# Kernel optimization log

Hardware: AMD Instinct MI355X
Metric: run time of the kernel (lower is better)

## Reference

```python
import jax, jax.numpy as jnp
import numpy as np

HEADS = 8
GROUPS = 32
EPS = 1e-5


def setup_inputs() -> dict:
    key = jax.random.key(0)
    k_x, k_qkv, k_proj = jax.random.split(key, 3)
    B, C, H, W = 16, 512, 32, 32
    s = 0.02  # init scale for weights
    return {
        "x": jax.random.normal(k_x, (B, C, H, W), jnp.float32),
        "gn_scale": jnp.ones((C,), jnp.float32),
        "gn_bias": jnp.zeros((C,), jnp.float32),
        "w_qkv": jax.random.normal(k_qkv, (3 * C, C), jnp.float32) * s,
        "b_qkv": jnp.zeros((3 * C,), jnp.float32),
        "w_proj": jax.random.normal(k_proj, (C, C), jnp.float32) * s,
        "b_proj": jnp.zeros((C,), jnp.float32),
    }


def _group_norm(x, scale, bias):
    # x: [B, C, T]; GroupNorm32 computes stats in fp32
    B, C, T = x.shape
    xg = x.reshape(B, GROUPS, C // GROUPS, T).astype(jnp.float32)
    mu = xg.mean(axis=(2, 3), keepdims=True)
    var = xg.var(axis=(2, 3), keepdims=True)
    xn = ((xg - mu) * jax.lax.rsqrt(var + EPS)).reshape(B, C, T)
    return xn * scale[None, :, None] + bias[None, :, None]


def reference(x, gn_scale, gn_bias, w_qkv, b_qkv, w_proj, b_proj):
    B, C = x.shape[0], x.shape[1]
    T = int(np.prod(x.shape[2:]))
    xf = x.reshape(B, C, T)
    xn = _group_norm(xf, gn_scale, gn_bias).astype(x.dtype)
    # 1x1 conv == per-position matmul: [B, 3C, T]
    qkv = jnp.einsum('oc,bct->bot', w_qkv, xn) + b_qkv[None, :, None]
    ch = C // HEADS
    qkv = qkv.reshape(B * HEADS, 3 * ch, T)
    q, k, v = jnp.split(qkv, 3, axis=1)  # each [B*H, ch, T]
    scale = ch ** -0.25
    # scores: [B*H, T, T], softmax in fp32 (matches weight.float())
    w = jnp.einsum('bct,bcs->bts', q * scale, k * scale)
    w = jax.nn.softmax(w.astype(jnp.float32), axis=-1).astype(q.dtype)
    a = jnp.einsum('bts,bcs->bct', w, v).reshape(B, C, T)
    h = jnp.einsum('oc,bct->bot', w_proj, a) + b_proj[None, :, None]
    return (xf + h).reshape(x.shape)
```

## Files before the change

### kernel.cpp

```cpp
#include <hip/hip_runtime.h>
#include <cstdint>

#define NB 16
#define NC 512
#define NT 1024
#define NH 8
#define NG 32
#define GN_EPS 1e-5f
#define KSOFT 0.18033688011112042f

typedef float  f32x16 __attribute__((ext_vector_type(16)));
typedef __bf16 bf16x8 __attribute__((ext_vector_type(8)));
typedef unsigned int uint32x4 __attribute__((ext_vector_type(4)));

static __device__ __forceinline__ f32x16 zero16() {
    f32x16 z;
    #pragma unroll
    for (int i = 0; i < 16; ++i) z[i] = 0.f;
    return z;
}

static __device__ __forceinline__ f32x16 mfma(bf16x8 a, bf16x8 b, f32x16 c) {
    return __builtin_amdgcn_mfma_f32_32x32x16_bf16(a, b, c, 0, 0, 0);
}

static __device__ __forceinline__ unsigned pk2(float a, float b) {
    unsigned short x = __builtin_bit_cast(unsigned short, (__bf16)a);
    unsigned short y = __builtin_bit_cast(unsigned short, (__bf16)b);
    return (unsigned)x | ((unsigned)y << 16);
}

static __device__ __forceinline__ void swap32(unsigned& a, unsigned& b) {
#if __has_builtin(__builtin_amdgcn_permlane32_swap)
    auto r = __builtin_amdgcn_permlane32_swap(a, b, false, false);
    a = r[0];
    b = r[1];
#else
    unsigned sa = __shfl_xor(a, 32), sb = __shfl_xor(b, 32);
    bool hi = (threadIdx.x & 32) != 0;
    unsigned na = hi ? sb : a;
    unsigned nb = hi ? b : sa;
    a = na; b = nb;
#endif
}

static __device__ __forceinline__ bf16x8 lds_frag(const __bf16* base, int row, int sb) {
    const char* p = (const char*)base + row * 128 + (sb ^ ((row & 7) << 4));
    return *(const bf16x8*)p;
}

#define GLOAD16(gp, lp)                                                        \
    __builtin_amdgcn_global_load_lds(                                          \
        (const __attribute__((address_space(1))) unsigned int*)(gp),           \
        (__attribute__((address_space(3))) unsigned int*)(lp), 16, 0, 0)

__global__ __launch_bounds__(256) void fused_pre(
        const float* __restrict__ x, const float* __restrict__ gs,
        const float* __restrict__ gb, const float* __restrict__ w_qkv,
        const float* __restrict__ w_proj, __bf16* __restrict__ xnT,
        __bf16* __restrict__ wq_bf, __bf16* __restrict__ wp_bf)
{
    const int blk = blockIdx.x;
    const int thr = threadIdx.x;
    if (blk >= 128) {
        int i = (blk - 128) * 256 + thr;
        const float* src;
        __bf16* dst;
        if (i < 196608) { src = w_qkv; dst = wq_bf; }
        else            { i -= 196608; src = w_proj; dst = wp_bf; }
        float4 f = ((const float4*)src)[i];
        uint2 u;
        u.x = pk2(f.x, f.y);
        u.y = pk2(f.z, f.w);
        ((uint2*)dst)[i] = u;
        return;
    }
    const int b = blk >> 3, c0 = (blk & 7) * 64;
    __shared__ float gstat[8];
    {
        const int wv = thr >> 6, lane = thr & 63;
        const float* base = x + ((size_t)b * NC + c0 + wv * 16) * NT;
        float s = 0.f, s2 = 0.f;
        #pragma unroll
        for (int ch = 0; ch < 16; ++ch) {
            const float4* r4 = (const float4*)(base + (size_t)ch * NT);
            #pragma unroll
            for (int p = 0; p < 4; ++p) {
                float4 v = r4[lane + p * 64];
                s += v.x + v.y + v.z + v.w;
                s2 = fmaf(v.x, v.x, fmaf(v.y, v.y, fmaf(v.z, v.z, fmaf(v.w, v.w, s2))));
            }
        }
        #pragma unroll
        for (int off = 32; off; off >>= 1) {
            s  += __shfl_down(s, off);
            s2 += __shfl_down(s2, off);
        }
        if (lane == 0) {
            const float inv_n = 1.f / 16384.f;
            float mu  = s * inv_n;
            float var = s2 * inv_n - mu * mu;
            gstat[wv]     = mu;
            gstat[wv + 4] = rsqrtf(var + GN_EPS);
        }
    }
    __syncthreads();
    __shared__ float xs[64][65];
    const int tloc = thr & 63;
    for (int t0 = 0; t0 < NT; t0 += 64) {
        #pragma unroll
        for (int p = 0; p < 16; ++p) {
            int cr = p * 4 + (thr >> 6);
            int c = c0 + cr;
            float mu = gstat[cr >> 4];
            float rs = gstat[(cr >> 4) + 4];
            float v = x[((size_t)b * NC + c) * NT + t0 + tloc];
            xs[cr][tloc] = (v - mu) * rs * gs[c] + gb[c];
        }
        __syncthreads();
        const int cd = thr & 31;
        #pragma unroll
        for (int pp = 0; pp < 8; ++pp) {
            int tr = pp * 8 + (thr >> 5);
            unsigned w = pk2(xs[2 * cd][tr], xs[2 * cd + 1][tr]);
            size_t off = ((size_t)b * NT + t0 + tr) * NC + c0 + 2 * cd;
            *(unsigned*)((char*)xnT + off * 2) = w;
        }
        __syncthreads();
    }
}

__global__ __launch_bounds__(256) void qkv_gemm(const __bf16* __restrict__ wq,
                                                const __bf16* __restrict__ xnT,
                                                const float* __restrict__ bias,
                                                __bf16* __restrict__ qv,
                                                __bf16* __restrict__ kT)
{
    const int b = blockIdx.z, o0 = blockIdx.y * 128, t0 = blockIdx.x * 128;
    __shared__ __align__(16) char smem[32768];
    __bf16* wt = (__bf16*)smem;
    __bf16* xt = (__bf16*)(smem + 16384);
    const int thr = threadIdx.x;
    const int lane = thr & 63, wv = thr >> 6;
    const int lr = lane & 31, h = lane >> 5;
    const int wo = (wv >> 1) * 64, wn = (wv & 1) * 64;
    f32x16 acc[2][2];
    #pragma unroll
    for (int i = 0; i < 2; ++i)
        #pragma unroll
        for (int j = 0; j < 2; ++j) acc[i][j] = zero16();

    for (int kb = 0; kb < 8; ++kb) {
        const int c0 = kb * 64;
        __syncthreads();
        #pragma unroll
        for (int p = 0; p < 4; ++p) {
            int idx = p * 256 + thr, row = idx >> 3, sl = idx & 7;
            GLOAD16(wq + (size_t)(o0 + row) * NC + c0 + 8 * (sl ^ (row & 7)), wt + idx * 8);
            GLOAD16(xnT + ((size_t)b * NT + t0 + row) * NC + c0 + 8 * (sl ^ (row & 7)), xt + idx * 8);
        }
        asm volatile("s_waitcnt vmcnt(0)" ::: "memory");
        __syncthreads();
        #pragma unroll
        for (int kc = 0; kc < 4; ++kc) {
            bf16x8 a0 = lds_frag(wt, wo + lr,      32 * kc + 16 * h);
            bf16x8 a1 = lds_frag(wt, wo + 32 + lr, 32 * kc + 16 * h);
            bf16x8 b0 = lds_frag(xt, wn + lr,      32 * kc + 16 * h);
            bf16x8 b1 = lds_frag(xt, wn + 32 + lr, 32 * kc + 16 * h);
            acc[0][0] = mfma(a0, b0, acc[0][0]);
            acc[0][1] = mfma(a0, b1, acc[0][1]);
            acc[1][0] = mfma(a1, b0, acc[1][0]);
            acc[1][1] = mfma(a1, b1, acc[1][1]);
        }
    }

    char* ktile = smem;
    #pragma unroll
    for (int mt = 0; mt < 2; ++mt) {
        const int X = o0 + wo + 32 * mt;
        const int xm = X % 192;
        const int cat = xm >> 6;
        const int hd = X / 192;
        if (cat != 1) {
            #pragma unroll
            for (int nt = 0; nt < 2; ++nt)
                #pragma unroll
                for (int r = 0; r < 16; ++r) {
                    int off = (r & 3) + 8 * (r >> 2) + 4 * h;
                    int o = X + off;
                    int row = (cat == 0) ? (xm + off) : (xm - 64 + off);
                    int t = t0 + wn + 32 * nt + lr;
                    float v = acc[mt][nt][r] + bias[o];
                    if (cat == 0) v *= KSOFT;
                    qv[((size_t)(b * 8 + hd) * 128 + row) * NT + t] = (__bf16)v;
                }
        }
    }
    __syncthreads();
    #pragma unroll
    for (int mt = 0; mt < 2; ++mt) {
        const int X = o0 + wo + 32 * mt;
        const int xm = X % 192;
        if ((xm >> 6) == 1) {
            #pragma unroll
            for (int nt = 0; nt < 2; ++nt) {
                int t_local = wn + 32 * nt + lr;
                #pragma unroll
                for (int g = 0; g < 4; ++g) {
                    int ob = X + 8 * g + 4 * h;
                    int cb = (xm - 64) + 8 * g + 4 * h;
                    uint2 d;
                    d.x = pk2(acc[mt][nt][4 * g + 0] + bias[ob + 0],
                              acc[mt][nt][4 * g + 1] + bias[ob + 1]);
                    d.y = pk2(acc[mt][nt][4 * g + 2] + bias[ob + 2],
                              acc[mt][nt][4 * g + 3] + bias[ob + 3]);
                    *(uint2*)(ktile + t_local * 144 + cb * 2) = d;
                }
            }
        }
    }
    if ((o0 % 192) != 128) {
        __syncthreads();
        const int khd = o0 / 192;
        #pragma unroll
        for (int pass = 0; pass < 4; ++pass) {
            int t_local = pass * 32 + (thr >> 3);
            int c8 = thr & 7;
            uint32x4 d = *(const uint32x4*)(ktile + t_local * 144 + c8 * 16);
            *(uint32x4*)(kT + ((size_t)(b * 8 + khd) * 1024 + t0 + t_local) * 64 + c8 * 8) = d;
        }
    }
}

#define PP(R) ((R) < 16 ? p0[(R) & 15] : p1[(R) & 15])

__global__ __launch_bounds__(512, 4) void attn_mfma(const __bf16* __restrict__ qv,
                                                    const __bf16* __restrict__ kT,
                                                    __bf16* __restrict__ aT)
{
    const int wg = blockIdx.x;
    const int orig = (wg & 7) * 64 + (wg >> 3);
    const int tq0 = (orig & 3) * 256;
    const int bh = orig >> 2;
    const int b = bh >> 3, hd = bh & 7;
    const __bf16* qg = qv + (size_t)bh * 128 * NT;
    const __bf16* vg = qg + (size_t)64 * NT;
    const __bf16* kTg = kT + (size_t)bh * 1024 * 64;
    const int thr = threadIdx.x, lane = thr & 63, wv = thr >> 6;
    const int lr = lane & 31, h = lane >> 5;
    const int tw = tq0 + wv * 32;
    __shared__ __align__(16) char smem[36864];
    __bf16* kb0 = (__bf16*)smem;
    __bf16* vb0 = (__bf16*)(smem + 8192);
    __bf16* kb1 = (__bf16*)(smem + 16384);
    __bf16* vb1 = (__bf16*)(smem + 24576);

    bf16x8 qf[4];
    {
        const unsigned short* qs = (const unsigned short*)qg;
        #pragma unroll
        for (int kc = 0; kc < 4; ++kc) {
            unsigned w[4];
            #pragma unroll
            for (int ww = 0; ww < 4; ++ww) {
                int c0 = 16 * kc + 8 * h + 2 * ww;
                unsigned lo = qs[(size_t)c0 * NT + tw + lr];
                unsigned hi = qs[(size_t)(c0 + 1) * NT + tw + lr];
                w[ww] = lo | (hi << 16);
            }
            uint32x4 u = {w[0], w[1], w[2], w[3]};
            qf[kc] = __builtin_bit_cast(bf16x8, u);
        }
    }
    bf16x8 ones;
    #pragma unroll
    for (int i = 0; i < 8; ++i) ones[i] = (__bf16)1.0f;

    f32x16 oacc0 = zero16(), oacc1 = zero16(), sacc = zero16();

    const int row = thr >> 3, sl = thr & 7;
    const __bf16* kbase = kTg + (size_t)row * 64 + 8 * (sl ^ (row & 7));
    const __bf16* vbase = vg + (size_t)row * NT + 8 * (sl ^ (row & 7));
    const int ldsoff = thr * 8;

    GLOAD16(kbase, kb0 + ldsoff);
    GLOAD16(vbase, vb0 + ldsoff);

    for (int it = 0; it < 16; ++it) {
        __bf16* kcur = (it & 1) ? kb1 : kb0;
        __bf16* vcur = (it & 1) ? vb1 : vb0;
        if (it < 15) {
            __bf16* knxt = (it & 1) ? kb0 : kb1;
            __bf16* vnxt = (it & 1) ? vb0 : vb1;
            const int s0 = (it + 1) * 64;
            GLOAD16(kbase + (size_t)s0 * 64, knxt + ldsoff);
            GLOAD16(vbase + s0, vnxt + ldsoff);
            asm volatile("s_waitcnt vmcnt(2)" ::: "memory");
        } else {
            asm volatile("s_waitcnt vmcnt(0)" ::: "memory");
        }
        __builtin_amdgcn_s_barrier();

        f32x16 p0 = zero16(), p1 = zero16();
        __builtin_amdgcn_s_setprio(1);
        #pragma unroll
        for (int kc = 0; kc < 4; ++kc) {
            bf16x8 ka0 = lds_frag(kcur, lr,      32 * kc + 16 * h);
            bf16x8 ka1 = lds_frag(kcur, 32 + lr, 32 * kc + 16 * h);
            p0 = mfma(ka0, qf[kc], p0);
            p1 = mfma(ka1, qf[kc], p1);
        }
        __builtin_amdgcn_s_setprio(0);

        #pragma unroll
        for (int r = 0; r < 16; ++r) {
            p0[r] = exp2f(p0[r]);
            p1[r] = exp2f(p1[r]);
        }

        #pragma unroll
        for (int ks = 0; ks < 4; ++ks) {
            const int Rb = 16 * (ks >> 1) + 8 * (ks & 1);
            unsigned a0 = pk2(PP(Rb + 0), PP(Rb + 1));
            unsigned c0 = pk2(PP(Rb + 2), PP(Rb + 3));
            unsigned a1 = pk2(PP(Rb + 4), PP(Rb + 5));
            unsigned c1 = pk2(PP(Rb + 6), PP(Rb + 7));
            swap32(a0, a1);
            swap32(c0, c1);
            uint32x4 u = {a0, c0, a1, c1};
            bf16x8 pf = __builtin_bit_cast(bf16x8, u);
            bf16x8 v0 = lds_frag(vcur, lr,      32 * ks + 16 * h);
            bf16x8 v1 = lds_frag(vcur, 32 + lr, 32 * ks + 16 * h);
            __builtin_amdgcn_s_setprio(1);
            oacc0 = mfma(v0, pf, oacc0);
            oacc1 = mfma(v1, pf, oacc1);
            sacc  = mfma(ones, pf, sacc);
            __builtin_amdgcn_s_setprio(0);
        }
        __builtin_amdgcn_s_barrier();
    }

    float inv = 1.f / sacc[0];
    char* at = smem;
    {
        int t_local = wv * 32 + lr;
        #pragma unroll
        for (int g = 0; g < 4; ++g) {
            int cb = 8 * g + 4 * h;
            uint2 d0, d1;
            d0.x = pk2(oacc0[4 * g + 0] * inv, oacc0[4 * g + 1] * inv);
            d0.y = pk2(oacc0[4 * g + 2] * inv, oacc0[4 * g + 3] * inv);
            *(uint2*)(at + t_local * 144 + cb * 2) = d0;
            d1.x = pk2(oacc1[4 * g + 0] * inv, oacc1[4 * g + 1] * inv);
            d1.y = pk2(oacc1[4 * g + 2] * inv, oacc1[4 * g + 3] * inv);
            *(uint2*)(at + t_local * 144 + (cb + 32) * 2) = d1;
        }
    }
    __syncthreads();
    #pragma unroll
    for (int pass = 0; pass < 4; ++pass) {
        int t_local = pass * 64 + (thr >> 3);
        int c8 = thr & 7;
        uint32x4 d = *(const uint32x4*)(at + t_local * 144 + c8 * 16);
        *(uint32x4*)(aT + ((size_t)b * NT + tq0 + t_local) * NC + hd * 64 + c8 * 8) = d;
    }
}

__global__ __launch_bounds__(256) void proj_gemm(const __bf16* __restrict__ wp,
                                                 const __bf16* __restrict__ aT,
                                                 const float* __restrict__ bias,
                                                 const float* __restrict__ x,
                                                 float* __restrict__ out)
{
    const int b = blockIdx.z, o0 = blockIdx.y * 128, t0 = blockIdx.x * 128;
    __shared__ __align__(16) char smem[32768];
    __bf16* wt = (__bf16*)smem;
    __bf16* xt = (__bf16*)(smem + 16384);
    const int thr = threadIdx.x;
    const int lane = thr & 63, wv = thr >> 6;
    const int lr = lane & 31, h = lane >> 5;
    const int wo = (wv >> 1) * 64, wn = (wv & 1) * 64;
    f32x16 acc[2][2];
    #pragma unroll
    for (int i = 0; i < 2; ++i)
        #pragma unroll
        for (int j = 0; j < 2; ++j) acc[i][j] = zero16();

    for (int kb = 0; kb < 8; ++kb) {
        const int c0 = kb * 64;
        __syncthreads();
        #pragma unroll
        for (int p = 0; p < 4; ++p) {
            int idx = p * 256 + thr, row = idx >> 3, sl = idx & 7;
            GLOAD16(wp + (size_t)(o0 + row) * NC + c0 + 8 * (sl ^ (row & 7)), wt + idx * 8);
            GLOAD16(aT + ((size_t)b * NT + t0 + row) * NC + c0 + 8 * (sl ^ (row & 7)), xt + idx * 8);
        }
        asm volatile("s_waitcnt vmcnt(0)" ::: "memory");
        __syncthreads();
        #pragma unroll
        for (int kc = 0; kc < 4; ++kc) {
            bf16x8 a0 = lds_frag(wt, wo + lr,      32 * kc + 16 * h);
            bf16x8 a1 = lds_frag(wt, wo + 32 + lr, 32 * kc + 16 * h);
            bf16x8 b0 = lds_frag(xt, wn + lr,      32 * kc + 16 * h);
            bf16x8 b1 = lds_frag(xt, wn + 32 + lr, 32 * kc + 16 * h);
            acc[0][0] = mfma(a0, b0, acc[0][0]);
            acc[0][1] = mfma(a0, b1, acc[0][1]);
            acc[1][0] = mfma(a1, b0, acc[1][0]);
            acc[1][1] = mfma(a1, b1, acc[1][1]);
        }
    }
    #pragma unroll
    for (int mt = 0; mt < 2; ++mt)
        #pragma unroll
        for (int nt = 0; nt < 2; ++nt)
            #pragma unroll
            for (int r = 0; r < 16; ++r) {
                int o = o0 + wo + 32 * mt + (r & 3) + 8 * (r >> 2) + 4 * h;
                int t = t0 + wn + 32 * nt + lr;
                size_t off = ((size_t)b * NC + o) * NT + t;
                out[off] = acc[mt][nt][r] + bias[o] + x[off];
            }
}

extern "C" void kernel_launch(void* const* d_in, const int* in_sizes, int n_in,
                              void* d_out, int out_size, void* d_ws, size_t ws_size,
                              hipStream_t stream)
{
    const float* x       = (const float*)d_in[0];
    const float* gnscale = (const float*)d_in[1];
    const float* gnbias  = (const float*)d_in[2];
    const float* w_qkv   = (const float*)d_in[3];
    const float* b_qkv   = (const float*)d_in[4];
    const float* w_proj  = (const float*)d_in[5];
    const float* b_proj  = (const float*)d_in[6];
    float* out = (float*)d_out;

    char* ws = (char*)d_ws;
    __bf16* wq_bf = (__bf16*)(ws + 4096);
    __bf16* wp_bf = (__bf16*)(ws + 1576960);
    __bf16* xnT   = (__bf16*)(ws + 2101248);
    __bf16* qv    = (__bf16*)(ws + 18878464);
    __bf16* kTb   = (__bf16*)(ws + 52432896);
    __bf16* aTb   = (__bf16*)(ws + 69210112);

    fused_pre<<<1152, 256, 0, stream>>>(x, gnscale, gnbias, w_qkv, w_proj,
                                        xnT, wq_bf, wp_bf);
    qkv_gemm<<<dim3(8, 12, NB), 256, 0, stream>>>(wq_bf, xnT, b_qkv, qv, kTb);
    attn_mfma<<<512, 512, 0, stream>>>(qv, kTb, aTb);
    proj_gemm<<<dim3(8, 4, NB), 256, 0, stream>>>(wp_bf, aTb, b_proj, x, out);
}
```

Before: 143.4 us.

## Double-buffer LDS tiles in QKV and projection GEMMs to overlap loads with MFMA

Both the QKV and output-projection GEMM kernels now keep two 32KB LDS stages. While the current k-block is computed, the next one is prefetched, and a partial vmcnt wait is used instead of a full drain, so global-to-LDS load latency is meant to hide behind MFMA work. This doubles LDS use to 64KB per block, which may cut occupancy. It also depends on the vmcnt(8) count matching the number of outstanding loads for correctness.

```diff
diff --git a/kernel.cpp b/kernel.cpp
--- a/kernel.cpp
+++ b/kernel.cpp
@@ -137,9 +137,7 @@
                                                 __bf16* __restrict__ kT)
 {
     const int b = blockIdx.z, o0 = blockIdx.y * 128, t0 = blockIdx.x * 128;
-    __shared__ __align__(16) char smem[32768];
-    __bf16* wt = (__bf16*)smem;
-    __bf16* xt = (__bf16*)(smem + 16384);
+    __shared__ __align__(16) char smem[65536];
     const int thr = threadIdx.x;
     const int lane = thr & 63, wv = thr >> 6;
     const int lr = lane & 31, h = lane >> 5;
@@ -150,17 +148,31 @@
         #pragma unroll
         for (int j = 0; j < 2; ++j) acc[i][j] = zero16();
 
+#define QKV_STAGE(c0v, wbuf, xbuf)                                             \
+    {                                                                          \
+        _Pragma("unroll")                                                      \
+        for (int p = 0; p < 4; ++p) {                                          \
+            int idx = p * 256 + thr, row = idx >> 3, sl = idx & 7;             \
+            GLOAD16(wq + (size_t)(o0 + row) * NC + (c0v) + 8 * (sl ^ (row & 7)), (wbuf) + idx * 8); \
+            GLOAD16(xnT + ((size_t)b * NT + t0 + row) * NC + (c0v) + 8 * (sl ^ (row & 7)), (xbuf) + idx * 8); \
+        }                                                                      \
+    }
+
+    QKV_STAGE(0, (__bf16*)smem, (__bf16*)(smem + 16384));
+
     for (int kb = 0; kb < 8; ++kb) {
-        const int c0 = kb * 64;
-        __syncthreads();
-        #pragma unroll
-        for (int p = 0; p < 4; ++p) {
-            int idx = p * 256 + thr, row = idx >> 3, sl = idx & 7;
-            GLOAD16(wq + (size_t)(o0 + row) * NC + c0 + 8 * (sl ^ (row & 7)), wt + idx * 8);
-            GLOAD16(xnT + ((size_t)b * NT + t0 + row) * NC + c0 + 8 * (sl ^ (row & 7)), xt + idx * 8);
-        }
-        asm volatile("s_waitcnt vmcnt(0)" ::: "memory");
-        __syncthreads();
+        const int cur = kb & 1;
+        __bf16* wt = (__bf16*)(smem + cur * 32768);
+        __bf16* xt = (__bf16*)(smem + cur * 32768 + 16384);
+        if (kb < 7) {
+            __bf16* wn2 = (__bf16*)(smem + (cur ^ 1) * 32768);
+            __bf16* xn2 = (__bf16*)(smem + (cur ^ 1) * 32768 + 16384);
+            QKV_STAGE((kb + 1) * 64, wn2, xn2);
+            asm volatile("s_waitcnt vmcnt(8)" ::: "memory");
+        } else {
+            asm volatile("s_waitcnt vmcnt(0)" ::: "memory");
+        }
+        __builtin_amdgcn_s_barrier();
         #pragma unroll
         for (int kc = 0; kc < 4; ++kc) {
             bf16x8 a0 = lds_frag(wt, wo + lr,      32 * kc + 16 * h);
@@ -172,6 +184,7 @@
             acc[1][0] = mfma(a1, b0, acc[1][0]);
             acc[1][1] = mfma(a1, b1, acc[1][1]);
         }
+        __builtin_amdgcn_s_barrier();
     }
 
     char* ktile = smem;
@@ -373,9 +386,7 @@
                                                  float* __restrict__ out)
 {
     const int b = blockIdx.z, o0 = blockIdx.y * 128, t0 = blockIdx.x * 128;
-    __shared__ __align__(16) char smem[32768];
-    __bf16* wt = (__bf16*)smem;
-    __bf16* xt = (__bf16*)(smem + 16384);
+    __shared__ __align__(16) char smem[65536];
     const int thr = threadIdx.x;
     const int lane = thr & 63, wv = thr >> 6;
     const int lr = lane & 31, h = lane >> 5;
@@ -386,17 +397,31 @@
         #pragma unroll
         for (int j = 0; j < 2; ++j) acc[i][j] = zero16();
 
+#define PROJ_STAGE(c0v, wbuf, xbuf)                                            \
+    {                                                                          \
+        _Pragma("unroll")                                                      \
+        for (int p = 0; p < 4; ++p) {                                          \
+            int idx = p * 256 + thr, row = idx >> 3, sl = idx & 7;             \
+            GLOAD16(wp + (size_t)(o0 + row) * NC + (c0v) + 8 * (sl ^ (row & 7)), (wbuf) + idx * 8); \
+            GLOAD16(aT + ((size_t)b * NT + t0 + row) * NC + (c0v) + 8 * (sl ^ (row & 7)), (xbuf) + idx * 8); \
+        }                                                                      \
+    }
+
+    PROJ_STAGE(0, (__bf16*)smem, (__bf16*)(smem + 16384));
+
     for (int kb = 0; kb < 8; ++kb) {
-        const int c0 = kb * 64;
-        __syncthreads();
-        #pragma unroll
-        for (int p = 0; p < 4; ++p) {
-            int idx = p * 256 + thr, row = idx >> 3, sl = idx & 7;
-            GLOAD16(wp + (size_t)(o0 + row) * NC + c0 + 8 * (sl ^ (row & 7)), wt + idx * 8);
-            GLOAD16(aT + ((size_t)b * NT + t0 + row) * NC + c0 + 8 * (sl ^ (row & 7)), xt + idx * 8);
-        }
-        asm volatile("s_waitcnt vmcnt(0)" ::: "memory");
-        __syncthreads();
+        const int cur = kb & 1;
+        __bf16* wt = (__bf16*)(smem + cur * 32768);
+        __bf16* xt = (__bf16*)(smem + cur * 32768 + 16384);
+        if (kb < 7) {
+            __bf16* wn2 = (__bf16*)(smem + (cur ^ 1) * 32768);
+            __bf16* xn2 = (__bf16*)(smem + (cur ^ 1) * 32768 + 16384);
+            PROJ_STAGE((kb + 1) * 64, wn2, xn2);
+            asm volatile("s_waitcnt vmcnt(8)" ::: "memory");
+        } else {
+            asm volatile("s_waitcnt vmcnt(0)" ::: "memory");
+        }
+        __builtin_amdgcn_s_barrier();
         #pragma unroll
         for (int kc = 0; kc < 4; ++kc) {
             bf16x8 a0 = lds_frag(wt, wo + lr,      32 * kc + 16 * h);
@@ -408,6 +433,7 @@
             acc[1][0] = mfma(a1, b0, acc[1][0]);
             acc[1][1] = mfma(a1, b1, acc[1][1]);
         }
+        __builtin_amdgcn_s_barrier();
     }
     #pragma unroll
     for (int mt = 0; mt < 2; ++mt)
```

Measured after the change: 152.1 us. +6.1%, slower.
